# Kernel tuning notes

Hardware: AMD Instinct MI355X
Metric: run time of the kernel (lower is better)

Reference implementation:

```python
import jax, jax.numpy as jnp
import numpy as np

N = 100_000   # nodes
E = 1_600_000 # edges
G = 64        # graphs in batch
IN_FEAT, H = 8, 16
NUM_CLASSES = 4


def _glorot(key, fi, fo):
    lim = float(np.sqrt(6.0 / (fi + fo)))
    return jax.random.uniform(key, (fi, fo), jnp.float32, -lim, lim)


def setup_inputs() -> dict:
    key = jax.random.key(0)
    ks = jax.random.split(key, 12)
    inp = {
        "x": jax.random.normal(ks[0], (N, IN_FEAT), jnp.float32),
        "edge_src": jax.random.randint(ks[1], (E,), 0, N, dtype=jnp.int32),
        "edge_dst": jax.random.randint(ks[2], (E,), 0, N, dtype=jnp.int32),
        "batch": jnp.sort(jax.random.randint(ks[3], (N,), 0, G, dtype=jnp.int32)),
    }
    dims = [(IN_FEAT, H), (H, 2 * H), (2 * H, 4 * H), (4 * H, 8 * H)]
    for i, (fi, fo) in enumerate(dims, 1):
        inp[f"W{i}"] = _glorot(ks[3 + i], fi, fo)
        inp[f"b{i}"] = jnp.zeros((fo,), jnp.float32)
    # PReLU slopes (torch default init 0.25, single parameter)
    inp["a1"] = jnp.float32(0.25)
    inp["a2"] = jnp.float32(0.25)
    inp["a3"] = jnp.float32(0.25)
    inp["Wlin"] = _glorot(ks[8], 8 * H, NUM_CLASSES)
    inp["blin"] = jnp.zeros((NUM_CLASSES,), jnp.float32)
    return inp


def _prelu(x, a):
    return jnp.where(x >= 0, x, a * x)


def reference(x, edge_src, edge_dst, batch,
              W1, b1, W2, b2, W3, b3, W4, b4,
              a1, a2, a3, Wlin, blin):
    # GCNConv: add self-loops, symmetric normalization D^-1/2 A_hat D^-1/2
    loops = jnp.arange(N, dtype=edge_src.dtype)
    src = jnp.concatenate([edge_src, loops])  # [E+N]
    dst = jnp.concatenate([edge_dst, loops])
    deg = jax.ops.segment_sum(jnp.ones_like(src, jnp.float32), dst, num_segments=N)
    dinv = jax.lax.rsqrt(jnp.maximum(deg, 1.0))
    norm = dinv[src] * dinv[dst]  # [E+N]

    def gcn(h, W, b):
        h = h @ W                                   # [N, Fout]
        msg = h[src] * norm[:, None]                # gather + edge scale
        return jax.ops.segment_sum(msg, dst, num_segments=N) + b

    h = _prelu(gcn(x, W1, b1), a1)
    h = _prelu(gcn(h, W2, b2), a2)
    h = _prelu(gcn(h, W3, b3), a3)
    h = gcn(h, W4, b4)

    # global mean pool over graphs
    sums = jax.ops.segment_sum(h, batch, num_segments=G)          # [G, 8H]
    cnts = jax.ops.segment_sum(jnp.ones((N,), jnp.float32), batch, num_segments=G)
    pooled = sums / jnp.maximum(cnts, 1.0)[:, None]
    # dropout(p=0.25) is identity at inference
    return pooled @ Wlin + blin                                    # [G, 4]
```

## Files before the change

### kernel.cpp

```cpp
#include <hip/hip_runtime.h>
#include <hip/hip_fp16.h>

#define NN 100000
#define NE 1600000
#define NG 64

#define BSHIFT 7
#define BUCKW (1 << BSHIFT)
#define NBUCK ((NN + BUCKW - 1) >> BSHIFT)
#define BIN_CHUNK 8192

union H8 { float4 f4; __half2 h2[4]; };
__device__ __forceinline__ void h8_to_f(const H8& h, float* f) {
    float2 a = __half22float2(h.h2[0]);
    float2 b = __half22float2(h.h2[1]);
    float2 c = __half22float2(h.h2[2]);
    float2 d = __half22float2(h.h2[3]);
    f[0]=a.x; f[1]=a.y; f[2]=b.x; f[3]=b.y; f[4]=c.x; f[5]=c.y; f[6]=d.x; f[7]=d.y;
}
__device__ __forceinline__ H8 f_to_h8(const float* f) {
    H8 h;
    h.h2[0] = __floats2half2_rn(f[0], f[1]);
    h.h2[1] = __floats2half2_rn(f[2], f[3]);
    h.h2[2] = __floats2half2_rn(f[4], f[5]);
    h.h2[3] = __floats2half2_rn(f[6], f[7]);
    return h;
}
__device__ __forceinline__ float prelu_f(float x, float s) {
    return fmaxf(x, 0.f) + s * fminf(x, 0.f);
}

__global__ __launch_bounds__(256) void bucket_hist_kernel(const int* __restrict__ dst,
                                                          int* __restrict__ bucket_cnt, int E) {
    __shared__ int h[NBUCK];
    for (int i = threadIdx.x; i < NBUCK; i += 256) h[i] = 0;
    __syncthreads();
    int stride = gridDim.x * 256;
    for (int e = blockIdx.x * 256 + threadIdx.x; e < E; e += stride)
        atomicAdd(&h[dst[e] >> BSHIFT], 1);
    __syncthreads();
    for (int i = threadIdx.x; i < NBUCK; i += 256)
        if (h[i]) atomicAdd(&bucket_cnt[i], h[i]);
}

__global__ void bucket_scan_kernel(const int* __restrict__ bcnt, int* __restrict__ boff,
                                   int* __restrict__ bcur) {
    __shared__ int buf[2][1024];
    int t = threadIdx.x;
    int v = (t < NBUCK) ? bcnt[t] : 0;
    buf[0][t] = v;
    __syncthreads();
    int cur = 0;
    for (int off = 1; off < 1024; off <<= 1) {
        int x = buf[cur][t];
        if (t >= off) x += buf[cur][t - off];
        buf[cur ^ 1][t] = x;
        __syncthreads();
        cur ^= 1;
    }
    if (t < NBUCK) {
        int e = buf[cur][t] - v;
        boff[t] = e;
        bcur[t] = e;
    }
}

__global__ __launch_bounds__(256) void bin_kernel(const int* __restrict__ src,
                                                  const int* __restrict__ dst,
                                                  int* __restrict__ bcur,
                                                  unsigned* __restrict__ binned, int E) {
    __shared__ int h[NBUCK];
    __shared__ int cur[NBUCK];
    for (int i = threadIdx.x; i < NBUCK; i += 256) h[i] = 0;
    __syncthreads();
    int base = blockIdx.x * BIN_CHUNK;
    int end = base + BIN_CHUNK; if (end > E) end = E;
    for (int e = base + threadIdx.x; e < end; e += 256)
        atomicAdd(&h[dst[e] >> BSHIFT], 1);
    __syncthreads();
    for (int i = threadIdx.x; i < NBUCK; i += 256) {
        int c = h[i];
        cur[i] = c ? atomicAdd(&bcur[i], c) : 0;
    }
    __syncthreads();
    for (int e = base + threadIdx.x; e < end; e += 256) {
        unsigned s = (unsigned)src[e], d = (unsigned)dst[e];
        int pos = atomicAdd(&cur[d >> BSHIFT], 1);
        binned[pos] = (s << BSHIFT) | (d & (BUCKW - 1));
    }
}

__global__ __launch_bounds__(256) void deg_dinv_kernel(const unsigned* __restrict__ binned,
                                                       const int* __restrict__ bucket_off,
                                                       const int* __restrict__ bucket_cnt,
                                                       int* __restrict__ deg,
                                                       float* __restrict__ dinv, int n) {
    __shared__ int ldeg[BUCKW];
    int b = blockIdx.x;
    for (int i = threadIdx.x; i < BUCKW; i += 256) ldeg[i] = 0;
    __syncthreads();
    int start = bucket_off[b], cnt = bucket_cnt[b];
    for (int k = threadIdx.x; k < cnt; k += 256)
        atomicAdd(&ldeg[binned[start + k] & (BUCKW - 1)], 1);
    __syncthreads();
    int v0 = b << BSHIFT;
    for (int i = threadIdx.x; i < BUCKW; i += 256) {
        int v = v0 + i;
        if (v < n) {
            int dg = ldeg[i];
            deg[v] = dg;
            dinv[v] = rsqrtf((float)dg + 1.0f);
        }
    }
}

__global__ void scan1_kernel(const int* __restrict__ cntin, int* __restrict__ excl,
                             int* __restrict__ bsum, int n) {
    __shared__ int buf[2][1024];
    int t = threadIdx.x;
    int gid = blockIdx.x * 1024 + t;
    int v = (gid < n) ? cntin[gid] : 0;
    buf[0][t] = v;
    __syncthreads();
    int cur = 0;
    for (int off = 1; off < 1024; off <<= 1) {
        int x = buf[cur][t];
        if (t >= off) x += buf[cur][t - off];
        buf[cur ^ 1][t] = x;
        __syncthreads();
        cur ^= 1;
    }
    int incl = buf[cur][t];
    if (gid < n) excl[gid] = incl - v;
    if (t == 1023) bsum[blockIdx.x] = incl;
}

__global__ void scan2_kernel(int* __restrict__ bsum, int nb) {
    __shared__ int buf[2][128];
    int t = threadIdx.x;
    int v = (t < nb) ? bsum[t] : 0;
    buf[0][t] = v;
    __syncthreads();
    int cur = 0;
    for (int off = 1; off < 128; off <<= 1) {
        int x = buf[cur][t];
        if (t >= off) x += buf[cur][t - off];
        buf[cur ^ 1][t] = x;
        __syncthreads();
        cur ^= 1;
    }
    if (t < nb) bsum[t] = buf[cur][t] - v;
}

__global__ void scan3_kernel(int* __restrict__ excl, const int* __restrict__ bsum, int n) {
    int gid = blockIdx.x * blockDim.x + threadIdx.x;
    if (gid < n) excl[gid] += bsum[gid >> 10];
}

__global__ __launch_bounds__(256) void build2_kernel(const unsigned* __restrict__ binned,
                                                     const int* __restrict__ bucket_off,
                                                     const int* __restrict__ bucket_cnt,
                                                     const int* __restrict__ roff,
                                                     int* __restrict__ csr_src, int n) {
    __shared__ int lcur[BUCKW];
    int b = blockIdx.x;
    int v0 = b << BSHIFT;
    for (int i = threadIdx.x; i < BUCKW; i += 256) {
        int v = v0 + i;
        lcur[i] = (v < n) ? roff[v] : 0;
    }
    __syncthreads();
    int start = bucket_off[b], cnt = bucket_cnt[b];
    for (int k = threadIdx.x; k < cnt; k += 256) {
        unsigned e = binned[start + k];
        int pos = atomicAdd(&lcur[e & (BUCKW - 1)], 1);
        csr_src[pos] = (int)(e >> BSHIFT);
    }
}

__global__ __launch_bounds__(256) void makeM_kernel(
    const float* __restrict__ W4, const float* __restrict__ b4,
    const float* __restrict__ Wlin, const float* __restrict__ blin,
    float* __restrict__ M, float* __restrict__ bb) {
    int t = threadIdx.x;
    int k = t >> 2, c = t & 3;
    float m = 0.f;
    for (int j = 0; j < 128; ++j) m += W4[k * 128 + j] * Wlin[j * 4 + c];
    M[k * 4 + c] = m;
    if (t < 4) {
        float v = blin[t];
        for (int j = 0; j < 128; ++j) v += b4[j] * Wlin[j * 4 + t];
        bb[t] = v;
    }
}

__global__ __launch_bounds__(256) void aggmm1_kernel(
    const float* __restrict__ x, const int* __restrict__ row_off,
    const int* __restrict__ deg, const float* __restrict__ dinv,
    const int* __restrict__ csr_src, const float* __restrict__ W1,
    const float* __restrict__ b1, const float* __restrict__ a1,
    float4* __restrict__ Aout, int n) {
    __shared__ float Wl[8 * 16];
    for (int i = threadIdx.x; i < 8 * 16; i += 256) Wl[i] = W1[i];
    __syncthreads();
    int idx = blockIdx.x * 256 + threadIdx.x;
    if (idx >= n * 2) return;
    int v = idx >> 1;
    int c = idx & 1;
    const float4* h4 = (const float4*)x;
    float dvv = dinv[v];
    float4 self = h4[(size_t)v * 2 + c];
    float4 acc = make_float4(self.x * dvv, self.y * dvv, self.z * dvv, self.w * dvv);
    int start = row_off[v], cnt = deg[v];
    const int* __restrict__ row = csr_src + start;
    int j = 0;
    for (; j + 4 <= cnt; j += 4) {
        int s0 = row[j], s1 = row[j + 1], s2 = row[j + 2], s3 = row[j + 3];
        float d0 = dinv[s0], d1 = dinv[s1], d2 = dinv[s2], d3 = dinv[s3];
        float4 a0 = h4[(size_t)s0 * 2 + c];
        float4 a1v = h4[(size_t)s1 * 2 + c];
        float4 a2 = h4[(size_t)s2 * 2 + c];
        float4 a3 = h4[(size_t)s3 * 2 + c];
        acc.x += (a0.x * d0 + a1v.x * d1) + (a2.x * d2 + a3.x * d3);
        acc.y += (a0.y * d0 + a1v.y * d1) + (a2.y * d2 + a3.y * d3);
        acc.z += (a0.z * d0 + a1v.z * d1) + (a2.z * d2 + a3.z * d3);
        acc.w += (a0.w * d0 + a1v.w * d1) + (a2.w * d2 + a3.w * d3);
    }
    for (; j < cnt; ++j) {
        int s = row[j];
        float ds = dinv[s];
        float4 a = h4[(size_t)s * 2 + c];
        acc.x += a.x * ds; acc.y += a.y * ds; acc.z += a.z * ds; acc.w += a.w * ds;
    }
    float t[4] = { acc.x * dvv, acc.y * dvv, acc.z * dvv, acc.w * dvv };
    float po[4];
#pragma unroll
    for (int k = 0; k < 4; ++k) po[k] = __shfl_xor(t[k], 1, 64);
    int ob = c * 8;
    int e0 = c * 4, e1 = 4 - e0;
    float accm[8];
#pragma unroll
    for (int q = 0; q < 8; ++q) accm[q] = b1[ob + q];
#pragma unroll
    for (int k = 0; k < 4; ++k) {
        float r1 = t[k], r2 = po[k];
        const float* w1 = &Wl[(e0 + k) * 16 + ob];
        const float* w2 = &Wl[(e1 + k) * 16 + ob];
#pragma unroll
        for (int q = 0; q < 8; ++q) accm[q] += r1 * w1[q] + r2 * w2[q];
    }
    float s = *a1;
    float o[8];
#pragma unroll
    for (int q = 0; q < 8; ++q) o[q] = prelu_f(accm[q], s) * dvv;
    H8 h = f_to_h8(o);
    Aout[(size_t)v * 2 + c] = h.f4;
}

__global__ __launch_bounds__(256) void aggmm2_kernel(
    const float4* __restrict__ hs, const int* __restrict__ row_off,
    const int* __restrict__ deg, const float* __restrict__ dinv,
    const int* __restrict__ csr_src, const float* __restrict__ W2,
    const float* __restrict__ b2, const float* __restrict__ a2,
    float4* __restrict__ Aout, int n) {
    __shared__ float Wl[16 * 32];
    for (int i = threadIdx.x; i < 16 * 32; i += 256) Wl[i] = W2[i];
    __syncthreads();
    int idx = blockIdx.x * 256 + threadIdx.x;
    if (idx >= n * 2) return;
    int v = idx >> 1;
    int c = idx & 1;
    float a[8];
    { H8 h; h.f4 = hs[(size_t)v * 2 + c]; h8_to_f(h, a); }
    int start = row_off[v], cnt = deg[v];
    const int* __restrict__ row = csr_src + start;
    int j = 0;
    for (; j + 8 <= cnt; j += 8) {
        H8 hh[8];
#pragma unroll
        for (int q = 0; q < 8; ++q) hh[q].f4 = hs[(size_t)row[j + q] * 2 + c];
#pragma unroll
        for (int q = 0; q < 8; ++q) {
            float f[8]; h8_to_f(hh[q], f);
#pragma unroll
            for (int k = 0; k < 8; ++k) a[k] += f[k];
        }
    }
    for (; j < cnt; ++j) {
        H8 h; h.f4 = hs[(size_t)row[j] * 2 + c];
        float f[8]; h8_to_f(h, f);
#pragma unroll
        for (int k = 0; k < 8; ++k) a[k] += f[k];
    }
    float dvv = dinv[v];
#pragma unroll
    for (int k = 0; k < 8; ++k) a[k] *= dvv;
    float pa[8];
#pragma unroll
    for (int k = 0; k < 8; ++k) pa[k] = __shfl_xor(a[k], 1, 64);
    int ob = c * 16;
    int e0 = c * 8, e1 = 8 - e0;
    float accm[16];
#pragma unroll
    for (int q = 0; q < 16; ++q) accm[q] = b2[ob + q];
#pragma unroll
    for (int k = 0; k < 8; ++k) {
        float r1 = a[k], r2 = pa[k];
        const float* w1 = &Wl[(e0 + k) * 32 + ob];
        const float* w2 = &Wl[(e1 + k) * 32 + ob];
#pragma unroll
        for (int q = 0; q < 16; ++q) accm[q] += r1 * w1[q] + r2 * w2[q];
    }
    float s = *a2;
    float o[16];
#pragma unroll
    for (int q = 0; q < 16; ++q) o[q] = prelu_f(accm[q], s) * dvv;
    H8 h0 = f_to_h8(o);
    H8 h1 = f_to_h8(o + 8);
    Aout[(size_t)v * 4 + c * 2 + 0] = h0.f4;
    Aout[(size_t)v * 4 + c * 2 + 1] = h1.f4;
}

__global__ __launch_bounds__(256) void aggmm3_kernel(
    const float4* __restrict__ hs, const int* __restrict__ row_off,
    const int* __restrict__ deg, const float* __restrict__ dinv,
    const int* __restrict__ csr_src, const float* __restrict__ W3,
    const float* __restrict__ b3, const float* __restrict__ a3,
    const float* __restrict__ M, float4* __restrict__ z, int n) {
    __shared__ float Wl[32 * 64];
    __shared__ float Ml[64 * 4];
    for (int i = threadIdx.x; i < 32 * 64; i += 256) Wl[i] = W3[i];
    if (threadIdx.x < 64 * 4 && threadIdx.x < 256) {  }
    for (int i = threadIdx.x; i < 64 * 4; i += 256) Ml[i] = M[i];
    __syncthreads();
    int idx = blockIdx.x * 256 + threadIdx.x;
    if (idx >= n * 4) return;
    int v = idx >> 2;
    int c = idx & 3;
    float a[8];
    { H8 h; h.f4 = hs[(size_t)v * 4 + c]; h8_to_f(h, a); }
    int start = row_off[v], cnt = deg[v];
    const int* __restrict__ row = csr_src + start;
    int j = 0;
    for (; j + 8 <= cnt; j += 8) {
        H8 hh[8];
#pragma unroll
        for (int q = 0; q < 8; ++q) hh[q].f4 = hs[(size_t)row[j + q] * 4 + c];
#pragma unroll
        for (int q = 0; q < 8; ++q) {
            float f[8]; h8_to_f(hh[q], f);
#pragma unroll
            for (int k = 0; k < 8; ++k) a[k] += f[k];
        }
    }
    for (; j < cnt; ++j) {
        H8 h; h.f4 = hs[(size_t)row[j] * 4 + c];
        float f[8]; h8_to_f(h, f);
#pragma unroll
        for (int k = 0; k < 8; ++k) a[k] += f[k];
    }
    float dvv = dinv[v];
#pragma unroll
    for (int k = 0; k < 8; ++k) a[k] *= dvv;
    int ob = c * 16;
    float accm[16];
#pragma unroll
    for (int q = 0; q < 16; ++q) accm[q] = b3[ob + q];
#pragma unroll
    for (int m = 0; m < 4; ++m) {
        float cur[8];
        if (m == 0) {
#pragma unroll
            for (int k = 0; k < 8; ++k) cur[k] = a[k];
        } else {
#pragma unroll
            for (int k = 0; k < 8; ++k) cur[k] = __shfl_xor(a[k], m, 64);
        }
        int eb = (c ^ m) * 8;
#pragma unroll
        for (int k = 0; k < 8; ++k) {
            float rk = cur[k];
            const float* wp = &Wl[(eb + k) * 64 + ob];
#pragma unroll
            for (int q = 0; q < 16; ++q) accm[q] += rk * wp[q];
        }
    }
    float s = *a3;
    float px = 0.f, py = 0.f, pz = 0.f, pw = 0.f;
#pragma unroll
    for (int q = 0; q < 16; ++q) {
        float o = prelu_f(accm[q], s) * dvv;
        const float* mp = &Ml[(ob + q) * 4];
        px += o * mp[0]; py += o * mp[1]; pz += o * mp[2]; pw += o * mp[3];
    }
#pragma unroll
    for (int mask = 1; mask <= 2; mask <<= 1) {
        px += __shfl_xor(px, mask, 64);
        py += __shfl_xor(py, mask, 64);
        pz += __shfl_xor(pz, mask, 64);
        pw += __shfl_xor(pw, mask, 64);
    }
    if (c == 0) z[v] = make_float4(px, py, pz, pw);
}

__global__ __launch_bounds__(256) void aggpool4_kernel(
    const float4* __restrict__ z, const int* __restrict__ row_off,
    const int* __restrict__ deg, const float* __restrict__ dinv,
    const int* __restrict__ csr_src, const int* __restrict__ batch,
    float* __restrict__ sums, float* __restrict__ cnt, int n) {
    __shared__ float lacc[NG * 4];
    __shared__ float lcnt[NG];
    int tid = threadIdx.x;
    if (tid < NG * 4) lacc[tid] = 0.f;
    if (tid < NG) lcnt[tid] = 0.f;
    __syncthreads();
    int v = blockIdx.x * 256 + tid;
    bool valid = (v < n);
    float cx = 0.f, cy = 0.f, cz = 0.f, cw = 0.f, rc = 0.f;
    int g = -1;
    if (valid) {
        float4 acc = z[v];
        int start = row_off[v], dcnt = deg[v];
        const int* __restrict__ row = csr_src + start;
        int j = 0;
        for (; j + 4 <= dcnt; j += 4) {
            float4 a0 = z[row[j]];
            float4 a1 = z[row[j + 1]];
            float4 a2 = z[row[j + 2]];
            float4 a3 = z[row[j + 3]];
            acc.x += (a0.x + a1.x) + (a2.x + a3.x);
            acc.y += (a0.y + a1.y) + (a2.y + a3.y);
            acc.z += (a0.z + a1.z) + (a2.z + a3.z);
            acc.w += (a0.w + a1.w) + (a2.w + a3.w);
        }
        for (; j < dcnt; ++j) {
            float4 a = z[row[j]];
            acc.x += a.x; acc.y += a.y; acc.z += a.z; acc.w += a.w;
        }
        float dv = dinv[v];
        cx = acc.x * dv; cy = acc.y * dv; cz = acc.z * dv; cw = acc.w * dv;
        rc = 1.f;
        g = batch[v];
    }
    int g0 = __shfl(g, 0, 64);
    if (__all(g == g0 || !valid)) {
#pragma unroll
        for (int mask = 32; mask >= 1; mask >>= 1) {
            cx += __shfl_xor(cx, mask, 64);
            cy += __shfl_xor(cy, mask, 64);
            cz += __shfl_xor(cz, mask, 64);
            cw += __shfl_xor(cw, mask, 64);
            rc += __shfl_xor(rc, mask, 64);
        }
        if ((tid & 63) == 0) {
            float* lp = &lacc[g0 * 4];
            atomicAdd(lp + 0, cx); atomicAdd(lp + 1, cy);
            atomicAdd(lp + 2, cz); atomicAdd(lp + 3, cw);
            atomicAdd(&lcnt[g0], rc);
        }
    } else if (valid) {
        float* lp = &lacc[g * 4];
        atomicAdd(lp + 0, cx); atomicAdd(lp + 1, cy);
        atomicAdd(lp + 2, cz); atomicAdd(lp + 3, cw);
        atomicAdd(&lcnt[g], 1.f);
    }
    __syncthreads();
    if (tid < NG * 4) {
        float val = lacc[tid];
        if (val != 0.f) atomicAdd(&sums[tid], val);
    }
    if (tid < NG) {
        float val = lcnt[tid];
        if (val != 0.f) atomicAdd(&cnt[tid], val);
    }
}

__global__ void head_kernel(const float* __restrict__ sums, const float* __restrict__ cnt,
                            const float* __restrict__ bb, float* __restrict__ out) {
    int t = threadIdx.x;
    int g = t >> 2, c = t & 3;
    out[t] = sums[t] / fmaxf(cnt[g], 1.f) + bb[c];
}

extern "C" void kernel_launch(void* const* d_in, const int* in_sizes, int n_in,
                              void* d_out, int out_size, void* d_ws, size_t ws_size,
                              hipStream_t stream) {
    const float* x    = (const float*)d_in[0];
    const int* esrc   = (const int*)d_in[1];
    const int* edst   = (const int*)d_in[2];
    const int* batch  = (const int*)d_in[3];
    const float* W1 = (const float*)d_in[4],  *b1 = (const float*)d_in[5];
    const float* W2 = (const float*)d_in[6],  *b2 = (const float*)d_in[7];
    const float* W3 = (const float*)d_in[8],  *b3 = (const float*)d_in[9];
    const float* W4 = (const float*)d_in[10], *b4 = (const float*)d_in[11];
    const float* a1 = (const float*)d_in[12];
    const float* a2 = (const float*)d_in[13];
    const float* a3 = (const float*)d_in[14];
    const float* Wlin = (const float*)d_in[15], *blin = (const float*)d_in[16];
    float* out = (float*)d_out;

    const int N = NN, E = NE;
    const int NB = (N + 1023) / 1024;
    const int NBIN = (E + BIN_CHUNK - 1) / BIN_CHUNK;

    char* w = (char*)d_ws;
    size_t off = 0;
    auto alloc = [&](size_t bytes) { size_t r = off; off += (bytes + 255) & ~(size_t)255; return r; };
    size_t o_bcnt = alloc((size_t)NBUCK * 4);
    size_t o_pool = alloc((size_t)NG * 4 * 4);
    size_t o_cnt  = alloc((size_t)NG * 4);
    size_t zero_bytes = off;
    size_t o_deg  = alloc((size_t)N * 4);
    size_t o_dinv = alloc((size_t)N * 4);
    size_t o_roff = alloc((size_t)N * 4);
    size_t o_boff = alloc((size_t)NBUCK * 4);
    size_t o_bcur = alloc((size_t)NBUCK * 4);
    size_t o_bsum = alloc((size_t)128 * 4);
    size_t o_csrc = alloc((size_t)E * 4);
    size_t o_bin  = alloc((size_t)E * 4);
    size_t o_A1   = alloc((size_t)N * 16 * 2);
    size_t o_A2   = alloc((size_t)N * 32 * 2);
    size_t o_z    = alloc((size_t)N * 4 * 4);
    size_t o_M    = alloc((size_t)64 * 4 * 4);
    size_t o_bb   = alloc((size_t)4 * 4);
    (void)ws_size;
    int*      bcnt   = (int*)(w + o_bcnt);
    float*    pool   = (float*)(w + o_pool);
    float*    cnt    = (float*)(w + o_cnt);
    int*      deg    = (int*)(w + o_deg);
    float*    dinv   = (float*)(w + o_dinv);
    int*      roff   = (int*)(w + o_roff);
    int*      boff   = (int*)(w + o_boff);
    int*      bcur   = (int*)(w + o_bcur);
    int*      bsum   = (int*)(w + o_bsum);
    int*      csrc   = (int*)(w + o_csrc);
    unsigned* binned = (unsigned*)(w + o_bin);
    float4*   A1     = (float4*)(w + o_A1);
    float4*   A2     = (float4*)(w + o_A2);
    float4*   z      = (float4*)(w + o_z);
    float*    M      = (float*)(w + o_M);
    float*    bb     = (float*)(w + o_bb);

    hipMemsetAsync(w, 0, zero_bytes, stream);

    makeM_kernel<<<1, 256, 0, stream>>>(W4, b4, Wlin, blin, M, bb);

    bucket_hist_kernel<<<256, 256, 0, stream>>>(edst, bcnt, E);
    bucket_scan_kernel<<<1, 1024, 0, stream>>>(bcnt, boff, bcur);
    bin_kernel<<<NBIN, 256, 0, stream>>>(esrc, edst, bcur, binned, E);
    deg_dinv_kernel<<<NBUCK, 256, 0, stream>>>(binned, boff, bcnt, deg, dinv, N);
    scan1_kernel<<<NB, 1024, 0, stream>>>(deg, roff, bsum, N);
    scan2_kernel<<<1, 128, 0, stream>>>(bsum, NB);
    scan3_kernel<<<(N + 255) / 256, 256, 0, stream>>>(roff, bsum, N);
    build2_kernel<<<NBUCK, 256, 0, stream>>>(binned, boff, bcnt, roff, csrc, N);

    aggmm1_kernel<<<(N * 2 + 255) / 256, 256, 0, stream>>>(
        x, roff, deg, dinv, csrc, W1, b1, a1, A1, N);

    aggmm2_kernel<<<(N * 2 + 255) / 256, 256, 0, stream>>>(
        A1, roff, deg, dinv, csrc, W2, b2, a2, A2, N);

    aggmm3_kernel<<<(N * 4 + 255) / 256, 256, 0, stream>>>(
        A2, roff, deg, dinv, csrc, W3, b3, a3, M, z, N);

    aggpool4_kernel<<<(N + 255) / 256, 256, 0, stream>>>(
        z, roff, deg, dinv, csrc, batch, pool, cnt, N);
    head_kernel<<<1, 256, 0, stream>>>(pool, cnt, bb, out);
}
```

Baseline: 258.3 us.

## Fuse degree, row-offset scan and CSR fill into one per-bucket kernel

Replaces the degree kernel, the three-stage global prefix scan and the CSR build kernel with a single per-bucket kernel. Row offsets come from the bucket offset plus a local shared-memory scan over the 128 nodes in the bucket. This removes four kernel launches and a second read of the binned edge array. The cost is a small in-block scan with extra barriers.

```diff
diff --git a/kernel.cpp b/kernel.cpp
--- a/kernel.cpp
+++ b/kernel.cpp
@@ -90,88 +90,49 @@
     }
 }
 
-__global__ __launch_bounds__(256) void deg_dinv_kernel(const unsigned* __restrict__ binned,
-                                                       const int* __restrict__ bucket_off,
-                                                       const int* __restrict__ bucket_cnt,
-                                                       int* __restrict__ deg,
-                                                       float* __restrict__ dinv, int n) {
+__global__ __launch_bounds__(256) void build_csr_kernel(
+    const unsigned* __restrict__ binned, const int* __restrict__ bucket_off,
+    const int* __restrict__ bucket_cnt, int* __restrict__ deg, float* __restrict__ dinv,
+    int* __restrict__ roff, int* __restrict__ csr_src, int n) {
     __shared__ int ldeg[BUCKW];
+    __shared__ int lscan[2][BUCKW];
+    __shared__ int lcur[BUCKW];
     int b = blockIdx.x;
-    for (int i = threadIdx.x; i < BUCKW; i += 256) ldeg[i] = 0;
+    int tid = threadIdx.x;
+    for (int i = tid; i < BUCKW; i += 256) ldeg[i] = 0;
     __syncthreads();
     int start = bucket_off[b], cnt = bucket_cnt[b];
-    for (int k = threadIdx.x; k < cnt; k += 256)
+    for (int k = tid; k < cnt; k += 256)
         atomicAdd(&ldeg[binned[start + k] & (BUCKW - 1)], 1);
     __syncthreads();
+    if (tid < BUCKW) lscan[0][tid] = ldeg[tid];
+    __syncthreads();
+    int cur = 0;
+    for (int off = 1; off < BUCKW; off <<= 1) {
+        int x = 0;
+        if (tid < BUCKW) {
+            x = lscan[cur][tid];
+            if (tid >= off) x += lscan[cur][tid - off];
+        }
+        __syncthreads();
+        if (tid < BUCKW) lscan[cur ^ 1][tid] = x;
+        __syncthreads();
+        cur ^= 1;
+    }
     int v0 = b << BSHIFT;
-    for (int i = threadIdx.x; i < BUCKW; i += 256) {
-        int v = v0 + i;
+    if (tid < BUCKW) {
+        int v = v0 + tid;
         if (v < n) {
-            int dg = ldeg[i];
+            int dg = ldeg[tid];
             deg[v] = dg;
             dinv[v] = rsqrtf((float)dg + 1.0f);
-        }
-    }
-}
-
-__global__ void scan1_kernel(const int* __restrict__ cntin, int* __restrict__ excl,
-                             int* __restrict__ bsum, int n) {
-    __shared__ int buf[2][1024];
-    int t = threadIdx.x;
-    int gid = blockIdx.x * 1024 + t;
-    int v = (gid < n) ? cntin[gid] : 0;
-    buf[0][t] = v;
-    __syncthreads();
-    int cur = 0;
-    for (int off = 1; off < 1024; off <<= 1) {
-        int x = buf[cur][t];
-        if (t >= off) x += buf[cur][t - off];
-        buf[cur ^ 1][t] = x;
-        __syncthreads();
-        cur ^= 1;
-    }
-    int incl = buf[cur][t];
-    if (gid < n) excl[gid] = incl - v;
-    if (t == 1023) bsum[blockIdx.x] = incl;
-}
-
-__global__ void scan2_kernel(int* __restrict__ bsum, int nb) {
-    __shared__ int buf[2][128];
-    int t = threadIdx.x;
-    int v = (t < nb) ? bsum[t] : 0;
-    buf[0][t] = v;
-    __syncthreads();
-    int cur = 0;
-    for (int off = 1; off < 128; off <<= 1) {
-        int x = buf[cur][t];
-        if (t >= off) x += buf[cur][t - off];
-        buf[cur ^ 1][t] = x;
-        __syncthreads();
-        cur ^= 1;
-    }
-    if (t < nb) bsum[t] = buf[cur][t] - v;
-}
-
-__global__ void scan3_kernel(int* __restrict__ excl, const int* __restrict__ bsum, int n) {
-    int gid = blockIdx.x * blockDim.x + threadIdx.x;
-    if (gid < n) excl[gid] += bsum[gid >> 10];
-}
-
-__global__ __launch_bounds__(256) void build2_kernel(const unsigned* __restrict__ binned,
-                                                     const int* __restrict__ bucket_off,
-                                                     const int* __restrict__ bucket_cnt,
-                                                     const int* __restrict__ roff,
-                                                     int* __restrict__ csr_src, int n) {
-    __shared__ int lcur[BUCKW];
-    int b = blockIdx.x;
-    int v0 = b << BSHIFT;
-    for (int i = threadIdx.x; i < BUCKW; i += 256) {
-        int v = v0 + i;
-        lcur[i] = (v < n) ? roff[v] : 0;
-    }
-    __syncthreads();
-    int start = bucket_off[b], cnt = bucket_cnt[b];
-    for (int k = threadIdx.x; k < cnt; k += 256) {
+            int r = start + lscan[cur][tid] - dg;
+            roff[v] = r;
+            lcur[tid] = r;
+        }
+    }
+    __syncthreads();
+    for (int k = tid; k < cnt; k += 256) {
         unsigned e = binned[start + k];
         int pos = atomicAdd(&lcur[e & (BUCKW - 1)], 1);
         csr_src[pos] = (int)(e >> BSHIFT);
@@ -330,7 +291,6 @@
     __shared__ float Wl[32 * 64];
     __shared__ float Ml[64 * 4];
     for (int i = threadIdx.x; i < 32 * 64; i += 256) Wl[i] = W3[i];
-    if (threadIdx.x < 64 * 4 && threadIdx.x < 256) {  }
     for (int i = threadIdx.x; i < 64 * 4; i += 256) Ml[i] = M[i];
     __syncthreads();
     int idx = blockIdx.x * 256 + threadIdx.x;
@@ -500,7 +460,6 @@
     float* out = (float*)d_out;
 
     const int N = NN, E = NE;
-    const int NB = (N + 1023) / 1024;
     const int NBIN = (E + BIN_CHUNK - 1) / BIN_CHUNK;
 
     char* w = (char*)d_ws;
@@ -515,7 +474,6 @@
     size_t o_roff = alloc((size_t)N * 4);
     size_t o_boff = alloc((size_t)NBUCK * 4);
     size_t o_bcur = alloc((size_t)NBUCK * 4);
-    size_t o_bsum = alloc((size_t)128 * 4);
     size_t o_csrc = alloc((size_t)E * 4);
     size_t o_bin  = alloc((size_t)E * 4);
     size_t o_A1   = alloc((size_t)N * 16 * 2);
@@ -532,7 +490,6 @@
     int*      roff   = (int*)(w + o_roff);
     int*      boff   = (int*)(w + o_boff);
     int*      bcur   = (int*)(w + o_bcur);
-    int*      bsum   = (int*)(w + o_bsum);
     int*      csrc   = (int*)(w + o_csrc);
     unsigned* binned = (unsigned*)(w + o_bin);
     float4*   A1     = (float4*)(w + o_A1);
@@ -548,11 +505,7 @@
     bucket_hist_kernel<<<256, 256, 0, stream>>>(edst, bcnt, E);
     bucket_scan_kernel<<<1, 1024, 0, stream>>>(bcnt, boff, bcur);
     bin_kernel<<<NBIN, 256, 0, stream>>>(esrc, edst, bcur, binned, E);
-    deg_dinv_kernel<<<NBUCK, 256, 0, stream>>>(binned, boff, bcnt, deg, dinv, N);
-    scan1_kernel<<<NB, 1024, 0, stream>>>(deg, roff, bsum, N);
-    scan2_kernel<<<1, 128, 0, stream>>>(bsum, NB);
-    scan3_kernel<<<(N + 255) / 256, 256, 0, stream>>>(roff, bsum, N);
-    build2_kernel<<<NBUCK, 256, 0, stream>>>(binned, boff, bcnt, roff, csrc, N);
+    build_csr_kernel<<<NBUCK, 256, 0, stream>>>(binned, boff, bcnt, deg, dinv, roff, csrc, N);
 
     aggmm1_kernel<<<(N * 2 + 255) / 256, 256, 0, stream>>>(
         x, roff, deg, dinv, csrc, W1, b1, a1, A1, N);
```

Result: faster. 248.4 us (-3.8%).
